# Kernel optimization log

Measured on AMD Instinct MI355X. Metric: run time of the kernel, lower is better.

The kernel has to match this reference:

```python
import jax, jax.numpy as jnp
import numpy as np

V, D, E, K = 8192, 128, 262144, 512

def _sqrtm_psd(A):
    # symmetric PSD matrix square root via eigendecomposition
    w, v = jnp.linalg.eigh(A)
    w = jnp.clip(w, 0.0)
    return (v * jnp.sqrt(w)) @ v.T


def setup_inputs() -> dict:
    key = jax.random.key(0)
    k1, k2, k3, k4 = jax.random.split(key, 4)
    inputs = jax.random.normal(k1, (V, D), dtype=jnp.float32) * 0.1
    # targets must be SPD (it is passed through sqrtm as a covariance)
    A = jax.random.normal(k2, (K, K), dtype=jnp.float32) / np.sqrt(K)
    targets = A @ A.T + 0.1 * jnp.eye(K, dtype=jnp.float32)
    edge_index = jax.random.randint(k3, (2, E), 0, V, dtype=jnp.int32)
    pmat = jax.random.normal(k4, (K, V), dtype=jnp.float32) / np.sqrt(V)
    return {"inputs": inputs, "targets": targets, "edge_index": edge_index, "pmat": pmat}


def reference(inputs, targets, edge_index, pmat):
    n = inputs.shape[0]
    i, j = edge_index[0], edge_index[1]
    # per-edge squared distance -> exp weight (vectorized gather-compute)
    d = jnp.sum((inputs[i] - inputs[j]) ** 2, axis=-1)  # [E]
    w = jnp.exp(-d)
    # W starts as identity (self loops give exp(0)=1, same as eye); symmetric scatter
    W = jnp.eye(n, dtype=inputs.dtype)
    W = W.at[i, j].set(w).at[j, i].set(w)
    deg = W.sum(axis=1)
    L = jnp.diag(deg) - W
    k = pmat.shape[0]
    L_adj = pmat @ L @ pmat.T + 1e-05 * jnp.eye(k, dtype=inputs.dtype)
    S1 = jnp.linalg.inv(L_adj)
    S0 = targets.astype(jnp.float32)
    S0_sqrt = _sqrtm_psd(S0)
    S_ = _sqrtm_psd(S0_sqrt @ S1 @ S0_sqrt)
    return jnp.trace(S1) + jnp.trace(S0) - 2.0 * jnp.trace(S_)
```

## Files before the change

kernel.cpp:

```cpp
#include <hip/hip_runtime.h>
#include <math.h>

#define VN 8192
#define DN 128
#define EN 262144
#define KD 512
#define KK (KD*KD)

#define S_SS_LADJ 0
#define S_INV_C1  1
#define S_SS_S0   2
#define S_INV_C0  3
#define S_QRT_C0  4
#define S_SS_G    5
#define S_INV_CG  6
#define S_QRT_CG  7
#define S_TR_X    8
#define S_TR_S0   9
#define S_TR_YG   10

typedef __attribute__((ext_vector_type(8))) __bf16 bf16x8;
typedef __attribute__((ext_vector_type(4))) float f32x4;

static __device__ __forceinline__ float waveReduceAdd(float v) {
#pragma unroll
  for (int o = 32; o; o >>= 1) v += __shfl_xor(v, o);
  return v;
}

static __device__ __forceinline__ ushort f2b(float f) {
  unsigned x = __float_as_uint(f);
  unsigned r = (x + 0x7fffu + ((x >> 16) & 1u)) >> 16;
  return (ushort)r;
}
static __device__ __forceinline__ float b2f(ushort u) {
  return __uint_as_float((unsigned)u << 16);
}


__global__ __launch_bounds__(256) void transpose_k(const float* __restrict__ in,
                                                   float* __restrict__ out) {
  __shared__ float s[32][33];
  int tx = threadIdx.x & 31, ty = threadIdx.x >> 5;
  int v0 = blockIdx.x * 32, k0 = blockIdx.y * 32;
  for (int r = ty; r < 32; r += 8) s[r][tx] = in[(size_t)(k0 + r) * VN + v0 + tx];
  __syncthreads();
  for (int r = ty; r < 32; r += 8) out[(size_t)(v0 + r) * KD + k0 + tx] = s[tx][r];
}

__global__ __launch_bounds__(256) void count_k(const float* __restrict__ x,
                                               const int* __restrict__ ei,
                                               int* __restrict__ ea, int* __restrict__ eb,
                                               float* __restrict__ ew,
                                               int* __restrict__ cnt,
                                               unsigned int* __restrict__ bitmap) {
  int e = (int)(((unsigned)blockIdx.x * 256u + threadIdx.x) >> 6);
  int lane = threadIdx.x & 63;
  if (e >= EN) return;
  int i = ei[e], j = ei[EN + e];
  int a = i < j ? i : j;
  int b = i < j ? j : i;
  int ok = 0;
  if (lane == 0) {
    if (i != j) {
      unsigned key = (unsigned)a * (unsigned)VN + (unsigned)b;
      unsigned m = 1u << (key & 31u);
      unsigned old = atomicOr(bitmap + (key >> 5), m);
      ok = (old & m) ? 0 : 1;
    }
  }
  ok = __shfl(ok, 0);
  if (!ok) { if (lane == 0) ea[e] = -1; return; }
  float d0 = x[a * DN + lane]      - x[b * DN + lane];
  float d1 = x[a * DN + 64 + lane] - x[b * DN + 64 + lane];
  float s = d0 * d0 + d1 * d1;
  s = waveReduceAdd(s);
  if (lane == 0) {
    ea[e] = a; eb[e] = b; ew[e] = expf(-s);
    atomicAdd(cnt + a, 1);
    atomicAdd(cnt + b, 1);
  }
}

__global__ __launch_bounds__(1024) void scan_k(const int* __restrict__ cnt,
                                               int* __restrict__ rowptr,
                                               int* __restrict__ cursor) {
  __shared__ int sd[1024];
  __shared__ int carry;
  int tid = threadIdx.x;
  if (tid == 0) { carry = 0; rowptr[0] = 0; }
  __syncthreads();
  for (int c = 0; c < VN / 1024; ++c) {
    int v = c * 1024 + tid;
    int xv = cnt[v];
    sd[tid] = xv;
    __syncthreads();
    for (int off = 1; off < 1024; off <<= 1) {
      int t = (tid >= off) ? sd[tid - off] : 0;
      __syncthreads();
      sd[tid] += t;
      __syncthreads();
    }
    int incl = sd[tid];
    int base = carry;
    rowptr[v + 1] = base + incl;
    cursor[v] = base + incl - xv;
    __syncthreads();
    if (tid == 1023) carry = base + incl;
    __syncthreads();
  }
}

__global__ __launch_bounds__(256) void fill_k(const int* __restrict__ ea, const int* __restrict__ eb,
                                              const float* __restrict__ ew,
                                              int* __restrict__ cursor,
                                              int* __restrict__ adjj, float* __restrict__ adjw) {
  int e = blockIdx.x * 256 + threadIdx.x;
  if (e >= EN) return;
  int a = ea[e];
  if (a < 0) return;
  int b = eb[e];
  float w = ew[e];
  int p = atomicAdd(cursor + a, 1); adjj[p] = b; adjw[p] = w;
  int q = atomicAdd(cursor + b, 1); adjj[q] = a; adjw[q] = w;
}

__global__ __launch_bounds__(512) void buildB_k(const float* __restrict__ pmatT,
                                                const int* __restrict__ rowptr,
                                                const int* __restrict__ adjj,
                                                const float* __restrict__ adjw,
                                                float* __restrict__ Bout) {
  int v = blockIdx.x;
  int k = threadIdx.x;
  int s = rowptr[v], e = rowptr[v + 1];
  float acc = 0.f, sw = 0.f;
  for (int p = s; p < e; ++p) {
    int jj = adjj[p];
    float w = adjw[p];
    acc += w * pmatT[(size_t)jj * KD + k];
    sw += w;
  }
  Bout[(size_t)v * KD + k] = sw * pmatT[(size_t)v * KD + k] - acc;
}

__global__ __launch_bounds__(256) void gemm_big_k(const float* __restrict__ A,
                                                  const float* __restrict__ B,
                                                  float* __restrict__ C) {
  __shared__ __align__(16) float As[32][34];
  __shared__ __align__(16) float Bs[32][34];
  int tid = threadIdx.x;
  int tx = tid & 15, ty = tid >> 4;
  int n0 = blockIdx.x * 32, m0 = blockIdx.y * 32;
  int kbase = blockIdx.z * (VN / 8);
  float a00 = 0.f, a01 = 0.f, a10 = 0.f, a11 = 0.f;
  for (int kt = kbase; kt < kbase + VN / 8; kt += 32) {
#pragma unroll
    for (int u = 0; u < 4; ++u) {
      int li = tid * 4 + u;
      int r = li >> 5, c = li & 31;
      As[c][r] = A[(size_t)(m0 + r) * VN + kt + c];
      Bs[r][c] = B[(size_t)(kt + r) * KD + n0 + c];
    }
    __syncthreads();
#pragma unroll
    for (int k = 0; k < 32; ++k) {
      float2 av = *(const float2*)&As[k][2 * ty];
      float2 bv = *(const float2*)&Bs[k][2 * tx];
      a00 += av.x * bv.x; a01 += av.x * bv.y;
      a10 += av.y * bv.x; a11 += av.y * bv.y;
    }
    __syncthreads();
  }
  int m = m0 + 2 * ty, n = n0 + 2 * tx;
  atomicAdd(&C[m * KD + n], a00);
  atomicAdd(&C[m * KD + n + 1], a01);
  atomicAdd(&C[(m + 1) * KD + n], a10);
  atomicAdd(&C[(m + 1) * KD + n + 1], a11);
}


struct SmemT { ushort a[2][64][40]; ushort b[2][64][40]; };

static __device__ __forceinline__ void mgemm_s(SmemT* sm,
    const float* Asl, const float* Bsl, const float* Dsl, float* Csl,
    float alpha, float beta, int wsplit) {
  const ushort* Ah = (const ushort*)(Asl + KK);
  const ushort* Al = Ah + KK;
  const ushort* Bh = (const ushort*)(Bsl + KK);
  const ushort* Bl = Bh + KK;
  int tid = threadIdx.x;
  int lane = tid & 63, wave = tid >> 6;
  int wr = wave >> 1, wc = wave & 1;
  int fr = lane & 15, fq = lane >> 4;
  int m0 = blockIdx.y * 64, n0 = blockIdx.x * 64;
  int sr = tid >> 2, skc = (tid & 3) * 8;
  f32x4 acc[2][2] = {};
  for (int kt = 0; kt < KD; kt += 32) {
    *(uint4*)&sm->a[0][sr][skc] = *(const uint4*)&Ah[(size_t)(m0 + sr) * KD + kt + skc];
    *(uint4*)&sm->a[1][sr][skc] = *(const uint4*)&Al[(size_t)(m0 + sr) * KD + kt + skc];
    *(uint4*)&sm->b[0][sr][skc] = *(const uint4*)&Bh[(size_t)(n0 + sr) * KD + kt + skc];
    *(uint4*)&sm->b[1][sr][skc] = *(const uint4*)&Bl[(size_t)(n0 + sr) * KD + kt + skc];
    __syncthreads();
    bf16x8 ah[2], al[2], bh[2], bl[2];
#pragma unroll
    for (int m = 0; m < 2; ++m) {
      ah[m] = *(const bf16x8*)&sm->a[0][wr * 32 + m * 16 + fr][fq * 8];
      al[m] = *(const bf16x8*)&sm->a[1][wr * 32 + m * 16 + fr][fq * 8];
    }
#pragma unroll
    for (int n = 0; n < 2; ++n) {
      bh[n] = *(const bf16x8*)&sm->b[0][wc * 32 + n * 16 + fr][fq * 8];
      bl[n] = *(const bf16x8*)&sm->b[1][wc * 32 + n * 16 + fr][fq * 8];
    }
#pragma unroll
    for (int m = 0; m < 2; ++m)
#pragma unroll
      for (int n = 0; n < 2; ++n) {
        acc[m][n] = __builtin_amdgcn_mfma_f32_16x16x32_bf16(ah[m], bh[n], acc[m][n], 0, 0, 0);
        acc[m][n] = __builtin_amdgcn_mfma_f32_16x16x32_bf16(ah[m], bl[n], acc[m][n], 0, 0, 0);
        acc[m][n] = __builtin_amdgcn_mfma_f32_16x16x32_bf16(al[m], bh[n], acc[m][n], 0, 0, 0);
      }
    __syncthreads();
  }
  ushort* Ch = (ushort*)(Csl + KK);
  ushort* Cl = Ch + KK;
#pragma unroll
  for (int m = 0; m < 2; ++m)
#pragma unroll
    for (int n = 0; n < 2; ++n) {
      int col = n0 + wc * 32 + n * 16 + fr;
#pragma unroll
      for (int j = 0; j < 4; ++j) {
        int row = m0 + wr * 32 + m * 16 + fq * 4 + j;
        float v = alpha * acc[m][n][j];
        if (beta != 0.f) v += beta * Dsl[row * KD + col];
        Csl[row * KD + col] = v;
        if (wsplit) {
          ushort h = f2b(v);
          Ch[row * KD + col] = h;
          Cl[row * KD + col] = f2b(v - b2f(h));
        }
      }
    }
}

__global__ __launch_bounds__(256) void bc3_k(const float* Za, const float* Ya, float* Pm,
                                             const float* Xa, const float* Ra,
                                             float* Xb, float* Rb) {
  __shared__ SmemT sm;
  int z = blockIdx.z;
  if (z == 0)      mgemm_s(&sm, Za, Ya, nullptr, Pm, 1.f, 0.f, 1);
  else if (z == 1) mgemm_s(&sm, Xa, Ra, Xa, Xb, 1.f, 1.f, 1);
  else             mgemm_s(&sm, Ra, Ra, nullptr, Rb, 1.f, 0.f, 1);
}

__global__ __launch_bounds__(256) void yz2_k(const float* Ya, const float* Za, const float* Pm,
                                             float* Yb, float* Zb) {
  __shared__ SmemT sm;
  if (blockIdx.z == 0) mgemm_s(&sm, Ya, Pm, Ya, Yb, -0.5f, 1.5f, 1);
  else                 mgemm_s(&sm, Pm, Za, Za, Zb, -0.5f, 1.5f, 1);
}

__global__ __launch_bounds__(256) void inv2_k(const float* Xa, const float* Ra,
                                              float* Xb, float* Rb) {
  __shared__ SmemT sm;
  if (blockIdx.z == 0) mgemm_s(&sm, Xa, Ra, Xa, Xb, 1.f, 1.f, 1);
  else                 mgemm_s(&sm, Ra, Ra, nullptr, Rb, 1.f, 0.f, 1);
}

__global__ __launch_bounds__(256) void pm1_k(const float* Za, const float* Ya, float* Pm) {
  __shared__ SmemT sm;
  mgemm_s(&sm, Za, Ya, nullptr, Pm, 1.f, 0.f, 1);
}

__global__ __launch_bounds__(256) void one_k(const float* A, const float* B, float* C,
                                             int wsplit) {
  __shared__ SmemT sm;
  mgemm_s(&sm, A, B, nullptr, C, 1.f, 0.f, wsplit);
}


__global__ __launch_bounds__(256) void sumsq_k(const float* __restrict__ A, int n,
                                               float* __restrict__ slot) {
  float s = 0.f;
  for (int i = blockIdx.x * 256 + threadIdx.x; i < n; i += gridDim.x * 256) {
    float v = A[i];
    s += v * v;
  }
  __shared__ float p[4];
  s = waveReduceAdd(s);
  if ((threadIdx.x & 63) == 0) p[threadIdx.x >> 6] = s;
  __syncthreads();
  if (threadIdx.x == 0) atomicAdd(slot, p[0] + p[1] + p[2] + p[3]);
}

__global__ __launch_bounds__(512) void trace_k(const float* __restrict__ A,
                                               float* __restrict__ slot) {
  float v = A[(size_t)threadIdx.x * KD + threadIdx.x];
  __shared__ float p[8];
  v = waveReduceAdd(v);
  if ((threadIdx.x & 63) == 0) p[threadIdx.x >> 6] = v;
  __syncthreads();
  if (threadIdx.x == 0) {
    float t = 0.f;
    for (int i = 0; i < 8; ++i) t += p[i];
    slot[0] = t;
  }
}

__global__ void derive_k(const float* __restrict__ in, float* __restrict__ o_rsqrt,
                         float* __restrict__ o_qroot) {
  float x = in[0];
  o_rsqrt[0] = 1.0f / sqrtf(x);
  if (o_qroot) o_qroot[0] = powf(x, 0.25f);
}

__global__ __launch_bounds__(256) void setid_const_k(float* __restrict__ C, float val) {
  int idx = blockIdx.x * 256 + threadIdx.x;
  int r = idx >> 9, c = idx & (KD - 1);
  C[idx] = (r == c) ? val : 0.0f;
}

__global__ __launch_bounds__(256) void initinv_split_k(const float* __restrict__ Ladj,
                                                       const float* __restrict__ s,
                                                       float* __restrict__ X,
                                                       float* __restrict__ R) {
  int idx = blockIdx.x * 256 + threadIdx.x;
  int r = idx >> 9, c = idx & (KD - 1);
  float cv = s[0];
  float id = (r == c) ? 1.f : 0.f;
  float xv = id * cv;
  float rv = id - cv * Ladj[idx];
  ushort* Xh = (ushort*)(X + KK); ushort* Xl = Xh + KK;
  ushort* Rh = (ushort*)(R + KK); ushort* Rl = Rh + KK;
  X[idx] = xv; ushort h = f2b(xv); Xh[idx] = h; Xl[idx] = f2b(xv - b2f(h));
  R[idx] = rv; h = f2b(rv);        Rh[idx] = h; Rl[idx] = f2b(rv - b2f(h));
}

__global__ __launch_bounds__(256) void setid_split_k(float* __restrict__ C, float val) {
  int idx = blockIdx.x * 256 + threadIdx.x;
  int r = idx >> 9, c = idx & (KD - 1);
  float v = (r == c) ? val : 0.0f;
  ushort* Chh = (ushort*)(C + KK); ushort* Cll = Chh + KK;
  C[idx] = v; ushort h = f2b(v); Chh[idx] = h; Cll[idx] = f2b(v - b2f(h));
}

__global__ __launch_bounds__(256) void scale_split_k(const float* __restrict__ A,
                                                     const float* __restrict__ s,
                                                     float* __restrict__ C) {
  int idx = blockIdx.x * 256 + threadIdx.x;
  float v = A[idx] * s[0];
  ushort* Chh = (ushort*)(C + KK); ushort* Cll = Chh + KK;
  C[idx] = v; ushort h = f2b(v); Chh[idx] = h; Cll[idx] = f2b(v - b2f(h));
}

__global__ __launch_bounds__(256) void sym_k(const float* __restrict__ G,
                                             float* __restrict__ Out) {
  int idx = blockIdx.x * 256 + threadIdx.x;
  int r = idx >> 9, c = idx & (KD - 1);
  Out[idx] = 0.5f * (G[idx] + G[c * KD + r]);
}

__global__ void final_k(const float* __restrict__ scal, float* __restrict__ out) {
  out[0] = scal[S_TR_X] + scal[S_TR_S0] - 2.0f * scal[S_QRT_CG] * scal[S_TR_YG];
}


extern "C" void kernel_launch(void* const* d_in, const int* in_sizes, int n_in,
                              void* d_out, int out_size, void* d_ws, size_t ws_size,
                              hipStream_t stream) {
  (void)in_sizes; (void)n_in; (void)out_size; (void)ws_size;
  const float* x    = (const float*)d_in[0];
  const float* S0   = (const float*)d_in[1];
  const int*   ei   = (const int*)d_in[2];
  const float* pmat = (const float*)d_in[3];
  float* out = (float*)d_out;
  char* ws = (char*)d_ws;

  const size_t MB = 1u << 20;
  unsigned* bitmap = (unsigned*)ws;
  float* Ladj = (float*)ws;
  float* Gs   = (float*)(ws + 1 * MB);
  float* pmatT = (float*)(ws + 8 * MB);
  float* Bm    = (float*)(ws + 24 * MB);
  float* SL[11];
  for (int i = 0; i < 11; ++i) SL[i] = (float*)(ws + 8 * MB + (size_t)i * 2 * MB);
  float *Xa = SL[0], *Xb = SL[1], *Ra = SL[2], *Rb = SL[3];
  float *Ya = SL[4], *Yb = SL[5], *Za = SL[6], *Zb = SL[7];
  float *Pm = SL[8], *S0h = SL[9], *TMP = SL[10];
  size_t off = 40 * MB;
  int*   ea    = (int*)(ws + off);   off += (size_t)EN * 4;
  int*   eb    = (int*)(ws + off);   off += (size_t)EN * 4;
  float* ew    = (float*)(ws + off); off += (size_t)EN * 4;
  int*   cnt   = (int*)(ws + off);   off += (size_t)VN * 4;
  int*  rowptr = (int*)(ws + off);   off += (size_t)(VN + 2) * 4;
  int*  cursor = (int*)(ws + off);   off += (size_t)VN * 4;
  int*   adjj  = (int*)(ws + off);   off += (size_t)2 * EN * 4;
  float* adjw  = (float*)(ws + off); off += (size_t)2 * EN * 4;
  float* scal  = (float*)(ws + off); off += 64 * 4;

  hipMemsetAsync(bitmap, 0, (size_t)VN * VN / 8, stream);
  hipMemsetAsync(cnt, 0, (size_t)VN * 4, stream);
  hipMemsetAsync(scal, 0, 64 * 4, stream);

  transpose_k<<<dim3(VN / 32, KD / 32), 256, 0, stream>>>(pmat, pmatT);
  count_k<<<EN / 4, 256, 0, stream>>>(x, ei, ea, eb, ew, cnt, bitmap);
  scan_k<<<1, 1024, 0, stream>>>(cnt, rowptr, cursor);
  fill_k<<<EN / 256, 256, 0, stream>>>(ea, eb, ew, cursor, adjj, adjw);
  buildB_k<<<VN, 512, 0, stream>>>(pmatT, rowptr, adjj, adjw, Bm);
  setid_const_k<<<KK / 256, 256, 0, stream>>>(Ladj, 1e-5f);
  gemm_big_k<<<dim3(16, 16, 8), 256, 0, stream>>>(pmat, Bm, Ladj);

  sumsq_k<<<256, 256, 0, stream>>>(Ladj, KK, &scal[S_SS_LADJ]);
  derive_k<<<1, 1, 0, stream>>>(&scal[S_SS_LADJ], &scal[S_INV_C1], nullptr);
  initinv_split_k<<<KK / 256, 256, 0, stream>>>(Ladj, &scal[S_INV_C1], Xa, Ra);

  sumsq_k<<<256, 256, 0, stream>>>(S0, KK, &scal[S_SS_S0]);
  derive_k<<<1, 1, 0, stream>>>(&scal[S_SS_S0], &scal[S_INV_C0], &scal[S_QRT_C0]);
  scale_split_k<<<KK / 256, 256, 0, stream>>>(S0, &scal[S_INV_C0], Ya);
  setid_split_k<<<KK / 256, 256, 0, stream>>>(Za, 1.0f);

  for (int r = 0; r < 16; ++r) {
    bc3_k<<<dim3(8, 8, 3), 256, 0, stream>>>(Za, Ya, Pm, Xa, Ra, Xb, Rb);
    yz2_k<<<dim3(8, 8, 2), 256, 0, stream>>>(Ya, Za, Pm, Yb, Zb);
    float* t = Xa; Xa = Xb; Xb = t;
    t = Ra; Ra = Rb; Rb = t;
    t = Ya; Ya = Yb; Yb = t;
    t = Za; Za = Zb; Zb = t;
  }
  for (int r = 0; r < 2; ++r) {
    inv2_k<<<dim3(8, 8, 2), 256, 0, stream>>>(Xa, Ra, Xb, Rb);
    float* t = Xa; Xa = Xb; Xb = t;
    t = Ra; Ra = Rb; Rb = t;
  }
  trace_k<<<1, 512, 0, stream>>>(Xa, &scal[S_TR_X]);
  scale_split_k<<<KK / 256, 256, 0, stream>>>(Ya, &scal[S_QRT_C0], S0h);
  trace_k<<<1, 512, 0, stream>>>(S0, &scal[S_TR_S0]);

  one_k<<<dim3(8, 8, 1), 256, 0, stream>>>(S0h, Xa, TMP, 1);
  one_k<<<dim3(8, 8, 1), 256, 0, stream>>>(TMP, S0h, Gs, 0);
  sym_k<<<KK / 256, 256, 0, stream>>>(Gs, TMP);
  sumsq_k<<<256, 256, 0, stream>>>(TMP, KK, &scal[S_SS_G]);
  derive_k<<<1, 1, 0, stream>>>(&scal[S_SS_G], &scal[S_INV_CG], &scal[S_QRT_CG]);
  scale_split_k<<<KK / 256, 256, 0, stream>>>(TMP, &scal[S_INV_CG], Ya);
  setid_split_k<<<KK / 256, 256, 0, stream>>>(Za, 1.0f);
  for (int r = 0; r < 22; ++r) {
    pm1_k<<<dim3(8, 8, 1), 256, 0, stream>>>(Za, Ya, Pm);
    yz2_k<<<dim3(8, 8, 2), 256, 0, stream>>>(Ya, Za, Pm, Yb, Zb);
    float* t = Ya; Ya = Yb; Yb = t;
    t = Za; Za = Zb; Zb = t;
  }
  trace_k<<<1, 512, 0, stream>>>(Ya, &scal[S_TR_YG]);

  final_k<<<1, 1, 0, stream>>>(scal, out);
}
```

Before: 1.610 ms.

## Finish Newton-Schulz and sqrt iterations with fp32 refinement steps and fewer iterations

Drops one Newton-Schulz inverse iteration and two Denman-Beavers sqrt iterations. It replaces the final split-bf16 matrix steps with plain fp32 SIMT GEMMs: a residual-based Newton refinement X(2I - L X), and last Y/Z updates for both square roots. The S0h computation loses its split-precision storage, and buildB_k's gather loop is unrolled by four with separate accumulators. The workspace is also laid out differently. The fp32 scalar GEMMs are slower per call than the MFMA path but more accurate, which is what allows fewer iterations overall.

```diff
diff --git a/kernel.cpp b/kernel.cpp
--- a/kernel.cpp
+++ b/kernel.cpp
@@ -133,14 +133,24 @@
   int v = blockIdx.x;
   int k = threadIdx.x;
   int s = rowptr[v], e = rowptr[v + 1];
-  float acc = 0.f, sw = 0.f;
-  for (int p = s; p < e; ++p) {
+  float a0 = 0.f, a1 = 0.f, a2 = 0.f, a3 = 0.f, sw = 0.f;
+  int p = s;
+  for (; p + 4 <= e; p += 4) {
+    int j0 = adjj[p], j1 = adjj[p + 1], j2 = adjj[p + 2], j3 = adjj[p + 3];
+    float w0 = adjw[p], w1 = adjw[p + 1], w2 = adjw[p + 2], w3 = adjw[p + 3];
+    a0 += w0 * pmatT[(size_t)j0 * KD + k];
+    a1 += w1 * pmatT[(size_t)j1 * KD + k];
+    a2 += w2 * pmatT[(size_t)j2 * KD + k];
+    a3 += w3 * pmatT[(size_t)j3 * KD + k];
+    sw += w0 + w1 + w2 + w3;
+  }
+  for (; p < e; ++p) {
     int jj = adjj[p];
     float w = adjw[p];
-    acc += w * pmatT[(size_t)jj * KD + k];
+    a0 += w * pmatT[(size_t)jj * KD + k];
     sw += w;
   }
-  Bout[(size_t)v * KD + k] = sw * pmatT[(size_t)v * KD + k] - acc;
+  Bout[(size_t)v * KD + k] = sw * pmatT[(size_t)v * KD + k] - (a0 + a1 + a2 + a3);
 }
 
 __global__ __launch_bounds__(256) void gemm_big_k(const float* __restrict__ A,
@@ -176,6 +186,65 @@
   atomicAdd(&C[m * KD + n + 1], a01);
   atomicAdd(&C[(m + 1) * KD + n], a10);
   atomicAdd(&C[(m + 1) * KD + n + 1], a11);
+}
+
+
+static __device__ __forceinline__ void g32_body(const float* __restrict__ A,
+                                                const float* __restrict__ B,
+                                                const float* __restrict__ Dm,
+                                                float* __restrict__ C,
+                                                float alpha, float beta) {
+  __shared__ __align__(16) float As[32][34];
+  __shared__ __align__(16) float Bs[32][34];
+  int tid = threadIdx.x;
+  int tx = tid & 15, ty = tid >> 4;
+  int n0 = blockIdx.x * 32, m0 = blockIdx.y * 32;
+  float a00 = 0.f, a01 = 0.f, a10 = 0.f, a11 = 0.f;
+  for (int kt = 0; kt < KD; kt += 32) {
+#pragma unroll
+    for (int u = 0; u < 4; ++u) {
+      int li = tid * 4 + u;
+      int r = li >> 5, c = li & 31;
+      As[c][r] = A[(m0 + r) * KD + kt + c];
+      Bs[r][c] = B[(kt + r) * KD + n0 + c];
+    }
+    __syncthreads();
+#pragma unroll
+    for (int k = 0; k < 32; ++k) {
+      float2 av = *(const float2*)&As[k][2 * ty];
+      float2 bv = *(const float2*)&Bs[k][2 * tx];
+      a00 += av.x * bv.x; a01 += av.x * bv.y;
+      a10 += av.y * bv.x; a11 += av.y * bv.y;
+    }
+    __syncthreads();
+  }
+  int m = m0 + 2 * ty, n = n0 + 2 * tx;
+  float d00 = 0.f, d01 = 0.f, d10 = 0.f, d11 = 0.f;
+  if (beta != 0.0f) {
+    d00 = Dm[m * KD + n];       d01 = Dm[m * KD + n + 1];
+    d10 = Dm[(m + 1) * KD + n]; d11 = Dm[(m + 1) * KD + n + 1];
+  }
+  C[m * KD + n]           = alpha * a00 + beta * d00;
+  C[m * KD + n + 1]       = alpha * a01 + beta * d01;
+  C[(m + 1) * KD + n]     = alpha * a10 + beta * d10;
+  C[(m + 1) * KD + n + 1] = alpha * a11 + beta * d11;
+}
+
+__global__ __launch_bounds__(256) void gemm_kk(const float* __restrict__ A,
+                                               const float* __restrict__ B,
+                                               const float* __restrict__ Dm,
+                                               float* __restrict__ C,
+                                               float alpha, float beta) {
+  g32_body(A, B, Dm, C, alpha, beta);
+}
+
+__global__ __launch_bounds__(256) void gemm_dual32(const float* A0, const float* B0,
+                                                   const float* D0, float* C0,
+                                                   const float* A1, const float* B1,
+                                                   const float* D1, float* C1,
+                                                   float alpha, float beta) {
+  if (blockIdx.z == 0) g32_body(A0, B0, D0, C0, alpha, beta);
+  else                 g32_body(A1, B1, D1, C1, alpha, beta);
 }
 
 
@@ -261,22 +330,9 @@
   else                 mgemm_s(&sm, Pm, Za, Za, Zb, -0.5f, 1.5f, 1);
 }
 
-__global__ __launch_bounds__(256) void inv2_k(const float* Xa, const float* Ra,
-                                              float* Xb, float* Rb) {
-  __shared__ SmemT sm;
-  if (blockIdx.z == 0) mgemm_s(&sm, Xa, Ra, Xa, Xb, 1.f, 1.f, 1);
-  else                 mgemm_s(&sm, Ra, Ra, nullptr, Rb, 1.f, 0.f, 1);
-}
-
 __global__ __launch_bounds__(256) void pm1_k(const float* Za, const float* Ya, float* Pm) {
   __shared__ SmemT sm;
   mgemm_s(&sm, Za, Ya, nullptr, Pm, 1.f, 0.f, 1);
-}
-
-__global__ __launch_bounds__(256) void one_k(const float* A, const float* B, float* C,
-                                             int wsplit) {
-  __shared__ SmemT sm;
-  mgemm_s(&sm, A, B, nullptr, C, 1.f, 0.f, wsplit);
 }
 
 
@@ -354,6 +410,13 @@
   C[idx] = v; ushort h = f2b(v); Chh[idx] = h; Cll[idx] = f2b(v - b2f(h));
 }
 
+__global__ __launch_bounds__(256) void scale32_k(const float* __restrict__ A,
+                                                 const float* __restrict__ s,
+                                                 float* __restrict__ C) {
+  int idx = blockIdx.x * 256 + threadIdx.x;
+  C[idx] = A[idx] * s[0];
+}
+
 __global__ __launch_bounds__(256) void sym_k(const float* __restrict__ G,
                                              float* __restrict__ Out) {
   int idx = blockIdx.x * 256 + threadIdx.x;
@@ -376,28 +439,28 @@
   const float* pmat = (const float*)d_in[3];
   float* out = (float*)d_out;
   char* ws = (char*)d_ws;
-
   const size_t MB = 1u << 20;
+  const size_t SLOT = 2 * MB;
+
   unsigned* bitmap = (unsigned*)ws;
-  float* Ladj = (float*)ws;
-  float* Gs   = (float*)(ws + 1 * MB);
   float* pmatT = (float*)(ws + 8 * MB);
   float* Bm    = (float*)(ws + 24 * MB);
+  float* Ladj  = (float*)(ws + 40 * MB);
+  float* Gs    = (float*)(ws + 41 * MB);
+  int*   ea     = (int*)(ws + 40 * MB);
+  int*   eb     = (int*)(ws + 41 * MB);
+  float* ew     = (float*)(ws + 42 * MB);
+  int*   adjj   = (int*)(ws + 43 * MB);
+  float* adjw   = (float*)(ws + 45 * MB);
+  int*   cnt    = (int*)(ws + 47 * MB);
+  int*   rowptr = (int*)(ws + 47 * MB + 64 * 1024);
+  int*   cursor = (int*)(ws + 47 * MB + 128 * 1024);
+  float* scal   = (float*)(ws + 47 * MB + 256 * 1024);
   float* SL[11];
-  for (int i = 0; i < 11; ++i) SL[i] = (float*)(ws + 8 * MB + (size_t)i * 2 * MB);
-  float *Xa = SL[0], *Xb = SL[1], *Ra = SL[2], *Rb = SL[3];
-  float *Ya = SL[4], *Yb = SL[5], *Za = SL[6], *Zb = SL[7];
+  for (int i = 0; i < 11; ++i) SL[i] = (float*)(ws + (size_t)i * SLOT);
+  float *Xa = SL[0], *Ra = SL[1], *Ya = SL[2], *Za = SL[3];
+  float *Xb = SL[4], *Rb = SL[5], *Yb = SL[6], *Zb = SL[7];
   float *Pm = SL[8], *S0h = SL[9], *TMP = SL[10];
-  size_t off = 40 * MB;
-  int*   ea    = (int*)(ws + off);   off += (size_t)EN * 4;
-  int*   eb    = (int*)(ws + off);   off += (size_t)EN * 4;
-  float* ew    = (float*)(ws + off); off += (size_t)EN * 4;
-  int*   cnt   = (int*)(ws + off);   off += (size_t)VN * 4;
-  int*  rowptr = (int*)(ws + off);   off += (size_t)(VN + 2) * 4;
-  int*  cursor = (int*)(ws + off);   off += (size_t)VN * 4;
-  int*   adjj  = (int*)(ws + off);   off += (size_t)2 * EN * 4;
-  float* adjw  = (float*)(ws + off); off += (size_t)2 * EN * 4;
-  float* scal  = (float*)(ws + off); off += 64 * 4;
 
   hipMemsetAsync(bitmap, 0, (size_t)VN * VN / 8, stream);
   hipMemsetAsync(cnt, 0, (size_t)VN * 4, stream);
@@ -420,7 +483,7 @@
   scale_split_k<<<KK / 256, 256, 0, stream>>>(S0, &scal[S_INV_C0], Ya);
   setid_split_k<<<KK / 256, 256, 0, stream>>>(Za, 1.0f);
 
-  for (int r = 0; r < 16; ++r) {
+  for (int r = 0; r < 15; ++r) {
     bc3_k<<<dim3(8, 8, 3), 256, 0, stream>>>(Za, Ya, Pm, Xa, Ra, Xb, Rb);
     yz2_k<<<dim3(8, 8, 2), 256, 0, stream>>>(Ya, Za, Pm, Yb, Zb);
     float* t = Xa; Xa = Xb; Xb = t;
@@ -428,29 +491,37 @@
     t = Ya; Ya = Yb; Yb = t;
     t = Za; Za = Zb; Zb = t;
   }
-  for (int r = 0; r < 2; ++r) {
-    inv2_k<<<dim3(8, 8, 2), 256, 0, stream>>>(Xa, Ra, Xb, Rb);
-    float* t = Xa; Xa = Xb; Xb = t;
-    t = Ra; Ra = Rb; Rb = t;
-  }
-  trace_k<<<1, 512, 0, stream>>>(Xa, &scal[S_TR_X]);
-  scale_split_k<<<KK / 256, 256, 0, stream>>>(Ya, &scal[S_QRT_C0], S0h);
+
+  float* U32  = Xb;
+  float* Xfin = Rb;
+  gemm_kk<<<dim3(16, 16), 256, 0, stream>>>(Ladj, Xa, nullptr, U32, 1.0f, 0.0f);
+  gemm_kk<<<dim3(16, 16), 256, 0, stream>>>(Xa, U32, Xa, Xfin, -1.0f, 2.0f);
+  trace_k<<<1, 512, 0, stream>>>(Xfin, &scal[S_TR_X]);
   trace_k<<<1, 512, 0, stream>>>(S0, &scal[S_TR_S0]);
 
-  one_k<<<dim3(8, 8, 1), 256, 0, stream>>>(S0h, Xa, TMP, 1);
-  one_k<<<dim3(8, 8, 1), 256, 0, stream>>>(TMP, S0h, Gs, 0);
+  gemm_kk<<<dim3(16, 16), 256, 0, stream>>>(Za, Ya, nullptr, Pm, 1.0f, 0.0f);
+  gemm_kk<<<dim3(16, 16), 256, 0, stream>>>(Ya, Pm, Ya, Yb, -0.5f, 1.5f);
+  scale32_k<<<KK / 256, 256, 0, stream>>>(Yb, &scal[S_QRT_C0], S0h);
+
+  gemm_kk<<<dim3(16, 16), 256, 0, stream>>>(S0h, Xfin, nullptr, TMP, 1.0f, 0.0f);
+  gemm_kk<<<dim3(16, 16), 256, 0, stream>>>(TMP, S0h, nullptr, Gs, 1.0f, 0.0f);
   sym_k<<<KK / 256, 256, 0, stream>>>(Gs, TMP);
   sumsq_k<<<256, 256, 0, stream>>>(TMP, KK, &scal[S_SS_G]);
   derive_k<<<1, 1, 0, stream>>>(&scal[S_SS_G], &scal[S_INV_CG], &scal[S_QRT_CG]);
   scale_split_k<<<KK / 256, 256, 0, stream>>>(TMP, &scal[S_INV_CG], Ya);
   setid_split_k<<<KK / 256, 256, 0, stream>>>(Za, 1.0f);
-  for (int r = 0; r < 22; ++r) {
+  for (int r = 0; r < 20; ++r) {
     pm1_k<<<dim3(8, 8, 1), 256, 0, stream>>>(Za, Ya, Pm);
     yz2_k<<<dim3(8, 8, 2), 256, 0, stream>>>(Ya, Za, Pm, Yb, Zb);
     float* t = Ya; Ya = Yb; Yb = t;
     t = Za; Za = Zb; Zb = t;
   }
-  trace_k<<<1, 512, 0, stream>>>(Ya, &scal[S_TR_YG]);
+  gemm_kk<<<dim3(16, 16), 256, 0, stream>>>(Za, Ya, nullptr, Pm, 1.0f, 0.0f);
+  gemm_dual32<<<dim3(16, 16, 2), 256, 0, stream>>>(Ya, Pm, Ya, Yb,
+                                                   Pm, Za, Za, Zb, -0.5f, 1.5f);
+  gemm_kk<<<dim3(16, 16), 256, 0, stream>>>(Zb, Yb, nullptr, Pm, 1.0f, 0.0f);
+  gemm_kk<<<dim3(16, 16), 256, 0, stream>>>(Yb, Pm, Yb, S0h, -0.5f, 1.5f);
+  trace_k<<<1, 512, 0, stream>>>(S0h, &scal[S_TR_YG]);
 
   final_k<<<1, 1, 0, stream>>>(scal, out);
 }
```

New measurement: 1.580 ms. Within noise of the previous version (-1.9%).
